# Kernel optimization log

Measured on AMD Instinct MI355X. Metric: run time of the kernel, lower is better.

## Reference

```python
import jax, jax.numpy as jnp
import numpy as np

N_HEAD = 16
N_KV_HEADS = 4
HEAD_SIZE = 128  # n_embd // n_head = 2048 // 16


def setup_inputs() -> dict:
    key = jax.random.key(0)
    k0, k1, k2 = jax.random.split(key, 3)
    B, T, C = 4, 2048, 2048
    kv_dim = N_KV_HEADS * HEAD_SIZE  # 512
    x = jax.random.normal(k0, (B, T, C), dtype=jnp.float32)
    W_attn = jax.random.normal(k1, (C, C + 2 * kv_dim), dtype=jnp.float32) * 0.02
    b_attn = jnp.zeros((C + 2 * kv_dim,), dtype=jnp.float32)
    W_proj = jax.random.normal(k2, (C, C), dtype=jnp.float32) * 0.02
    b_proj = jnp.zeros((C,), dtype=jnp.float32)
    return {"x": x, "W_attn": W_attn, "b_attn": b_attn, "W_proj": W_proj, "b_proj": b_proj}


def reference(x, W_attn, b_attn, W_proj, b_proj):
    B, T, C = x.shape
    hs = HEAD_SIZE
    kv_dim = N_KV_HEADS * hs
    qkv = x @ W_attn + b_attn                      # [B,T,C+2*kv_dim]
    q, k, v = jnp.split(qkv, [C, C + kv_dim], axis=2)
    q = q.reshape(B, T, N_HEAD, hs).transpose(0, 2, 1, 3)       # [B,H,T,hs]
    k = k.reshape(B, T, N_KV_HEADS, hs).transpose(0, 2, 1, 3)   # [B,Hkv,T,hs]
    v = v.reshape(B, T, N_KV_HEADS, hs).transpose(0, 2, 1, 3)
    # GQA: repeat_interleave kv heads to match query heads
    rep = N_HEAD // N_KV_HEADS
    k_r = jnp.repeat(k, rep, axis=1)               # [B,H,T,hs]
    v_r = jnp.repeat(v, rep, axis=1)
    scale = 1.0 / jnp.sqrt(jnp.float32(hs))
    scores = jnp.einsum('bhqd,bhkd->bhqk', q, k_r) * scale      # [B,H,T,T]
    causal = jnp.tril(jnp.ones((T, T), dtype=bool))
    scores = jnp.where(causal, scores, jnp.finfo(scores.dtype).min)
    attn = jax.nn.softmax(scores, axis=-1)
    y = jnp.einsum('bhqk,bhkd->bhqd', attn, v_r)   # [B,H,T,hs]
    y = y.transpose(0, 2, 1, 3).reshape(B, T, C)
    y = y @ W_proj + b_proj
    return y
```

## Files before the change

### kernel.cpp

```cpp
#include <hip/hip_runtime.h>
#include <stdint.h>

#define DEVI __device__ __forceinline__

typedef __attribute__((ext_vector_type(8))) uint16_t u16x8;
typedef __attribute__((ext_vector_type(4))) uint16_t u16x4v;
typedef __attribute__((ext_vector_type(4))) uint32_t u32x4;
typedef __attribute__((ext_vector_type(8))) __bf16 bf16x8;
typedef __attribute__((ext_vector_type(4))) float f32x4;
typedef __attribute__((ext_vector_type(16))) float f32x16;

DEVI uint16_t f2bf(float x) {
  union { float f; uint32_t u; } v; v.f = x;
  return (uint16_t)((v.u + 0x7fffu + ((v.u >> 16) & 1u)) >> 16);
}

DEVI uint16_t f2bfn(float f) {
  __bf16 h = (__bf16)f;
  return __builtin_bit_cast(uint16_t, h);
}

DEVI f32x4 mfma16(u16x8 a, u16x8 b, f32x4 c) {
  return __builtin_amdgcn_mfma_f32_16x16x32_bf16(
      __builtin_bit_cast(bf16x8, a), __builtin_bit_cast(bf16x8, b), c, 0, 0, 0);
}

DEVI f32x16 mfma32(u16x8 a, u16x8 b, f32x16 c) {
  return __builtin_amdgcn_mfma_f32_32x32x16_bf16(
      __builtin_bit_cast(bf16x8, a), __builtin_bit_cast(bf16x8, b), c, 0, 0, 0);
}

DEVI void async16(void* lds, const void* g) {
  __builtin_amdgcn_global_load_lds(
      (const __attribute__((address_space(1))) uint32_t*)g,
      (__attribute__((address_space(3))) uint32_t*)lds, 16, 0, 0);
}

#define QSC 0.12751742925f

__global__ void cvt_f32_bf16(const float* __restrict__ in, uint16_t* __restrict__ out, int n4) {
  int i = blockIdx.x * blockDim.x + threadIdx.x;
  const int st = gridDim.x * blockDim.x;
  for (; i < n4; i += st) {
    float4 v = ((const float4*)in)[i];
    u16x4v o;
    o[0] = f2bf(v.x); o[1] = f2bf(v.y); o[2] = f2bf(v.z); o[3] = f2bf(v.w);
    ((u16x4v*)out)[i] = o;
  }
}

__global__ void transp_cvt(const float* __restrict__ in, uint16_t* __restrict__ out,
                           int K, int N) {
  __shared__ float Ws[64][65];
  const int n0 = blockIdx.x * 64, k0 = blockIdx.y * 64;
  const int t = threadIdx.x;
  const int r = t >> 4, c = (t & 15) << 2;
#pragma unroll
  for (int it = 0; it < 4; ++it) {
    float4 v = *(const float4*)&in[(size_t)(k0 + it * 16 + r) * N + n0 + c];
    Ws[it * 16 + r][c] = v.x; Ws[it * 16 + r][c + 1] = v.y;
    Ws[it * 16 + r][c + 2] = v.z; Ws[it * 16 + r][c + 3] = v.w;
  }
  __syncthreads();
#pragma unroll
  for (int it = 0; it < 4; ++it) {
    const int rr = it * 16 + r;
    const int cc = c;
    ushort4 o;
    o.x = f2bf(Ws[cc][rr]);     o.y = f2bf(Ws[cc + 1][rr]);
    o.z = f2bf(Ws[cc + 2][rr]); o.w = f2bf(Ws[cc + 3][rr]);
    *(ushort4*)&out[(size_t)(n0 + rr) * K + k0 + cc] = o;
  }
}

__global__ __launch_bounds__(512, 1)
void gemm_qkv(const uint16_t* __restrict__ A, const uint16_t* __restrict__ Bt,
              const float* __restrict__ bias,
              uint16_t* __restrict__ q, uint16_t* __restrict__ kk, uint16_t* __restrict__ vt,
              int M, int N, int K) {
  constexpr int BK = 64;
  __shared__ uint16_t As[2][256 * BK];
  __shared__ uint16_t Bs[2][192 * BK];
  int bid = (int)blockIdx.x;
  const int q8 = (int)gridDim.x >> 3;
  bid = (bid & 7) * q8 + (bid >> 3);
  const int nbn = N / 192;
  const int brow = (bid / nbn) << 8;
  const int bcol = (bid % nbn) * 192;
  const int t = threadIdx.x;
  const int wid = t >> 6, lane = t & 63;
  const int wm = wid >> 1, wn = wid & 1;
  const int lr = lane & 15, g = lane >> 4, l7 = lr & 7;

  const int logch = (((t & 7) ^ ((t >> 3) & 7)) << 3);
  const uint16_t* Asrc = A + (size_t)(brow + (t >> 3)) * K + logch;
  const uint16_t* Bsrc = Bt + (size_t)(bcol + (t >> 3)) * K + logch;
  const size_t skip64 = (size_t)64 * K;
  const int dt = t * 8;

  auto stageA = [&](int buf, int k0) {
#pragma unroll
    for (int l = 0; l < 4; ++l)
      async16(&As[buf][l * 4096 + dt], Asrc + (size_t)l * skip64 + k0);
  };
  auto stageB = [&](int buf, int k0) {
#pragma unroll
    for (int l = 0; l < 3; ++l)
      async16(&Bs[buf][l * 4096 + dt], Bsrc + (size_t)l * skip64 + k0);
  };

  f32x4 acc[4][6];
#pragma unroll
  for (int i = 0; i < 4; ++i)
#pragma unroll
    for (int j = 0; j < 6; ++j) acc[i][j] = f32x4{0.f, 0.f, 0.f, 0.f};

  const int nt = K / BK;
  stageA(0, 0); stageB(0, 0);
  if (nt > 1) { stageA(1, BK); stageB(1, BK); }
  asm volatile("s_waitcnt vmcnt(0)" ::: "memory");
  __builtin_amdgcn_s_barrier();

  for (int tt = 0; tt < nt; ++tt) {
    const int buf = tt & 1;
    u16x8 bfr[6][2], af[4][2];
#pragma unroll
    for (int j = 0; j < 6; ++j) {
      const int brw = wn * 96 + j * 16 + lr;
#pragma unroll
      for (int s = 0; s < 2; ++s)
        bfr[j][s] = *(const u16x8*)&Bs[buf][brw * 64 + ((((s << 2) + g) ^ l7) << 3)];
    }
#pragma unroll
    for (int ii = 0; ii < 4; ++ii) {
      const int arow = wm * 64 + ii * 16 + lr;
#pragma unroll
      for (int s = 0; s < 2; ++s)
        af[ii][s] = *(const u16x8*)&As[buf][arow * 64 + ((((s << 2) + g) ^ l7) << 3)];
    }
    asm volatile("s_waitcnt lgkmcnt(0)" ::: "memory");
    __builtin_amdgcn_sched_barrier(0);
    __builtin_amdgcn_s_barrier();
    if (tt + 2 < nt) {
      stageA(buf, (tt + 2) * BK);
      stageB(buf, (tt + 2) * BK);
      asm volatile("s_waitcnt vmcnt(7)" ::: "memory");
    } else {
      asm volatile("s_waitcnt vmcnt(0)" ::: "memory");
    }
    __builtin_amdgcn_s_setprio(1);
#pragma unroll
    for (int ii = 0; ii < 4; ++ii)
#pragma unroll
      for (int j = 0; j < 6; ++j)
#pragma unroll
        for (int s = 0; s < 2; ++s)
          acc[ii][j] = mfma16(af[ii][s], bfr[j][s], acc[ii][j]);
    __builtin_amdgcn_s_setprio(0);
    __builtin_amdgcn_s_barrier();
  }

#pragma unroll
  for (int i = 0; i < 4; ++i) {
#pragma unroll
    for (int j = 0; j < 6; ++j) {
      const int col = bcol + wn * 96 + j * 16 + lr;
      const float bb = bias[col];
      const int rowb = brow + wm * 64 + i * 16 + (g << 2);
      const int b_ = rowb >> 11, ttb = rowb & 2047;
      const int d = col & 127;
      float vals[4];
#pragma unroll
      for (int r = 0; r < 4; ++r) vals[r] = acc[i][j][r] + bb;
      if (col < 2048) {
        const int hh = col >> 7;
#pragma unroll
        for (int r = 0; r < 4; ++r)
          q[((size_t)((b_ * 16 + hh) * 2048 + ttb + r) << 7) + d] = f2bf(vals[r] * QSC);
      } else if (col < 2560) {
        const int hh = (col - 2048) >> 7;
#pragma unroll
        for (int r = 0; r < 4; ++r)
          kk[((size_t)((b_ * 4 + hh) * 2048 + ttb + r) << 7) + d] = f2bf(vals[r]);
      } else {
        const int hh = (col - 2560) >> 7;
        u16x4v pk;
#pragma unroll
        for (int r = 0; r < 4; ++r) pk[r] = f2bf(vals[r]);
        *(u16x4v*)&vt[(((size_t)((b_ * 4 + hh) * 128 + d)) << 11) + ttb] = pk;
      }
    }
  }
}

__global__ __launch_bounds__(512, 1)
void gemm_proj(const uint16_t* __restrict__ A, const uint16_t* __restrict__ Bt,
               const float* __restrict__ bias, float* __restrict__ outF,
               int M, int N, int K) {
  constexpr int BK = 64;
  __shared__ uint16_t As[2][256 * BK];
  __shared__ uint16_t Bs[2][256 * BK];
  int bid = (int)blockIdx.x;
  const int q8 = (int)gridDim.x >> 3;
  bid = (bid & 7) * q8 + (bid >> 3);
  const int nbn = N >> 8;
  const int brow = (bid / nbn) << 8;
  const int bcol = (bid % nbn) << 8;
  const int t = threadIdx.x;
  const int wid = t >> 6, lane = t & 63;
  const int wm = wid >> 2, wn = wid & 3;
  const int lr = lane & 15, g = lane >> 4;
  const int l7 = lr & 7;

  const int sr0 = t >> 3;
  const int logch = (((t & 7) ^ ((t >> 3) & 7)) << 3);
  const uint16_t* Asrc0 = A + (size_t)(brow + sr0) * K + logch;
  const uint16_t* Asrc1 = A + (size_t)(brow + 64 + sr0) * K + logch;
  const uint16_t* Bsrc0 = Bt + (size_t)(bcol + sr0) * K + logch;
  const uint16_t* Bsrc1 = Bt + (size_t)(bcol + 64 + sr0) * K + logch;
  const size_t hskip = (size_t)128 * K;
  const int d0 = t * 8, d1 = 4096 + t * 8;

  auto stageA = [&](int buf, int k0) {
    async16(&As[buf][d0], Asrc0 + k0);
    async16(&As[buf][d1], Asrc1 + k0);
    async16(&As[buf][8192 + d0], Asrc0 + hskip + k0);
    async16(&As[buf][8192 + d1], Asrc1 + hskip + k0);
  };
  auto stageB = [&](int buf, int k0) {
    async16(&Bs[buf][d0], Bsrc0 + k0);
    async16(&Bs[buf][d1], Bsrc1 + k0);
    async16(&Bs[buf][8192 + d0], Bsrc0 + hskip + k0);
    async16(&Bs[buf][8192 + d1], Bsrc1 + hskip + k0);
  };

  f32x4 acc[8][4];
#pragma unroll
  for (int i = 0; i < 8; ++i)
#pragma unroll
    for (int j = 0; j < 4; ++j) acc[i][j] = f32x4{0.f, 0.f, 0.f, 0.f};

  const int nt = K / BK;
  stageA(0, 0); stageB(0, 0);
  if (nt > 1) stageB(1, BK);
  asm volatile("s_waitcnt vmcnt(0)" ::: "memory");
  __builtin_amdgcn_s_barrier();

  for (int tt = 0; tt < nt; ++tt) {
    const int buf = tt & 1;
    u16x8 bfr[4][2];
#pragma unroll
    for (int p = 0; p < 2; ++p) {
      if (p == 0) {
#pragma unroll
        for (int j = 0; j < 4; ++j) {
          const int brw = wn * 64 + j * 16 + lr;
#pragma unroll
          for (int s = 0; s < 2; ++s)
            bfr[j][s] = *(const u16x8*)&Bs[buf][brw * 64 + ((((s << 2) + g) ^ l7) << 3)];
        }
      }
      u16x8 af[4][2];
#pragma unroll
      for (int ii = 0; ii < 4; ++ii) {
        const int arow = wm * 128 + (p * 4 + ii) * 16 + lr;
#pragma unroll
        for (int s = 0; s < 2; ++s)
          af[ii][s] = *(const u16x8*)&As[buf][arow * 64 + ((((s << 2) + g) ^ l7) << 3)];
      }
      if (p == 0) {
        if (tt + 1 < nt) stageA(buf ^ 1, (tt + 1) * BK);
      } else {
        if (tt + 2 < nt) {
          stageB(buf, (tt + 2) * BK);
          asm volatile("s_waitcnt vmcnt(4)" ::: "memory");
        } else {
          asm volatile("s_waitcnt vmcnt(0)" ::: "memory");
        }
      }
      __builtin_amdgcn_s_barrier();
      __builtin_amdgcn_s_setprio(1);
#pragma unroll
      for (int ii = 0; ii < 4; ++ii)
#pragma unroll
        for (int j = 0; j < 4; ++j)
#pragma unroll
          for (int s = 0; s < 2; ++s)
            acc[p * 4 + ii][j] = mfma16(af[ii][s], bfr[j][s], acc[p * 4 + ii][j]);
      __builtin_amdgcn_s_setprio(0);
      __builtin_amdgcn_s_barrier();
    }
  }

#pragma unroll
  for (int i = 0; i < 8; ++i) {
#pragma unroll
    for (int j = 0; j < 4; ++j) {
      const int col = bcol + wn * 64 + j * 16 + lr;
      const float bb = bias[col];
#pragma unroll
      for (int r = 0; r < 4; ++r) {
        const int row = brow + wm * 128 + i * 16 + (g << 2) + r;
        outF[(size_t)row * N + col] = acc[i][j][r] + bb;
      }
    }
  }
}

__global__ __launch_bounds__(512, 1)
void attn_fwd(const uint16_t* __restrict__ Q,
              const uint16_t* __restrict__ Kg,
              const uint16_t* __restrict__ Vt,
              uint16_t* __restrict__ Y,
              int T) {
  __shared__ __align__(16) uint16_t Ks[2][64 * 128];
  __shared__ __align__(16) uint16_t Vs[128 * 64];
  const int id = (int)blockIdx.x;
  const int x = id & 7;
  const int h = (id >> 3) & 15, b = (id >> 7) & 3;
  const int qb = (id & 256) ? 7 - x : x;
  const int hkv = h >> 2;

  const int t = threadIdx.x, w = t >> 6, lane = t & 63;
  const int ql = lane & 31, b5 = lane >> 5;
  const int swzK = (ql & 15) << 3;
  const int swzV = (ql & 7) << 3;

  const uint16_t* Qp = Q + ((size_t)(b * 16 + h) * T + qb * 256) * 128;
  const uint16_t* Kp = Kg + (size_t)(b * 4 + hkv) * T * 128;
  const uint16_t* Vp = Vt + (size_t)(b * 4 + hkv) * 128 * T;

  auto stageK = [&](int buf, int kv0) {
#pragma unroll
    for (int l = 0; l < 2; ++l) {
      const int s = l * 512 + t;
      const int row = s >> 4;
      const int cl = (s & 15) ^ (row & 15);
      async16(&Ks[buf][s * 8], &Kp[(size_t)(kv0 + row) * 128 + cl * 8]);
    }
  };
  auto stageV = [&](int kv0) {
#pragma unroll
    for (int l = 0; l < 2; ++l) {
      const int s = l * 512 + t;
      const int row = s >> 3;
      const int cl = (s & 7) ^ (row & 7);
      async16(&Vs[s * 8], &Vp[(size_t)row * T + kv0 + cl * 8]);
    }
  };

  const int row0 = qb * 256 + w * 32;
  const int qrow = row0 + ql;

  u16x8 qf[8];
#pragma unroll
  for (int kc = 0; kc < 8; ++kc)
    qf[kc] = *(const u16x8*)&Qp[(size_t)(w * 32 + ql) * 128 + kc * 16 + b5 * 8];

  f32x16 o[4];
#pragma unroll
  for (int db = 0; db < 4; ++db)
#pragma unroll
    for (int r = 0; r < 16; ++r) o[db][r] = 0.f;
  float mrow = -3e38f, lrow = 0.f;

  const int ntiles = 4 * qb + 4;
  const int myn = 4 * qb + (w >> 1) + 1;

  stageK(0, 0);
  __syncthreads();

  int cur = 0;
  for (int tile = 0; tile < ntiles; ++tile) {
    const int kv0 = tile << 6;
    stageV(kv0);
    if (tile + 1 < ntiles) stageK(cur ^ 1, (tile + 1) << 6);

    const bool run = tile < myn;
    f32x16 s[2];
    u16x8 pa[4];
    if (run) {
#pragma unroll
      for (int m = 0; m < 2; ++m)
#pragma unroll
        for (int r = 0; r < 16; ++r) s[m][r] = 0.f;
      __builtin_amdgcn_s_setprio(1);
#pragma unroll
      for (int kc = 0; kc < 8; ++kc) {
        const int cc = (kc * 16 + b5 * 8) ^ swzK;
        u16x8 k0f = *(const u16x8*)&Ks[cur][ql * 128 + cc];
        u16x8 k1f = *(const u16x8*)&Ks[cur][(32 + ql) * 128 + cc];
        s[0] = mfma32(k0f, qf[kc], s[0]);
        s[1] = mfma32(k1f, qf[kc], s[1]);
      }
      __builtin_amdgcn_s_setprio(0);

      if (kv0 + 63 > row0) {
#pragma unroll
        for (int m = 0; m < 2; ++m)
#pragma unroll
          for (int r = 0; r < 16; ++r) {
            const int kg = kv0 + 32 * m + (r & 3) + 8 * (r >> 2) + 4 * b5;
            if (kg > qrow) s[m][r] = -3e38f;
          }
      }
      float mt[16];
#pragma unroll
      for (int r = 0; r < 16; ++r) mt[r] = fmaxf(s[0][r], s[1][r]);
#pragma unroll
      for (int st = 8; st >= 1; st >>= 1)
#pragma unroll
        for (int r = 0; r < st; ++r) mt[r] = fmaxf(mt[r], mt[r + st]);
      float mx = fmaxf(mt[0], __shfl_xor(mt[0], 32));
      const bool defer = __all(mx <= mrow + 8.f);
      const float mnew = defer ? mrow : fmaxf(mrow, mx);
      const float sc = defer ? 1.f : exp2f(mrow - mnew);
#pragma unroll
      for (int m = 0; m < 2; ++m)
#pragma unroll
        for (int r = 0; r < 16; ++r) s[m][r] = exp2f(s[m][r] - mnew);
      float pt[16];
#pragma unroll
      for (int r = 0; r < 16; ++r) pt[r] = s[0][r] + s[1][r];
#pragma unroll
      for (int st = 8; st >= 1; st >>= 1)
#pragma unroll
        for (int r = 0; r < st; ++r) pt[r] += pt[r + st];
      float ps = pt[0] + __shfl_xor(pt[0], 32);
      mrow = mnew;
      lrow = lrow * sc + ps;
      if (!defer) {
#pragma unroll
        for (int db = 0; db < 4; ++db)
#pragma unroll
          for (int r = 0; r < 16; ++r) o[db][r] *= sc;
      }

#pragma unroll
      for (int m = 0; m < 2; ++m) {
        uint32_t pw[4][2];
#pragma unroll
        for (int a = 0; a < 4; ++a)
#pragma unroll
          for (int hh = 0; hh < 2; ++hh)
            pw[a][hh] = (uint32_t)f2bfn(s[m][4 * a + 2 * hh]) |
                        ((uint32_t)f2bfn(s[m][4 * a + 2 * hh + 1]) << 16);
#pragma unroll
        for (int c = 0; c < 2; ++c) {
          uint32_t wd[4];
#pragma unroll
          for (int hh = 0; hh < 2; ++hh) {
            const uint32_t mine  = b5 ? pw[2 * c + 1][hh] : pw[2 * c][hh];
            const uint32_t yours = b5 ? pw[2 * c][hh] : pw[2 * c + 1][hh];
            const uint32_t xw = (uint32_t)__shfl_xor((int)yours, 32);
            wd[hh] = b5 ? xw : mine;
            wd[2 + hh] = b5 ? mine : xw;
          }
          u32x4 tmp = {wd[0], wd[1], wd[2], wd[3]};
          pa[2 * m + c] = __builtin_bit_cast(u16x8, tmp);
        }
      }
    }
    __syncthreads();

    if (run) {
      __builtin_amdgcn_s_setprio(1);
#pragma unroll
      for (int db = 0; db < 4; ++db) {
#pragma unroll
        for (int kf = 0; kf < 4; ++kf) {
          u16x8 vf = *(const u16x8*)&Vs[(32 * db + ql) * 64 +
                                        ((kf * 16 + b5 * 8) ^ swzV)];
          o[db] = mfma32(vf, pa[kf], o[db]);
        }
      }
      __builtin_amdgcn_s_setprio(0);
    }
    __syncthreads();
    cur ^= 1;
  }

  uint16_t* Yp = Y + ((size_t)(b * T + row0 + ql)) * 2048 + h * 128 + b5 * 4;
  const float inv = 1.f / lrow;
#pragma unroll
  for (int db = 0; db < 4; ++db)
#pragma unroll
    for (int a = 0; a < 4; ++a) {
      u16x4v pk;
#pragma unroll
      for (int r = 0; r < 4; ++r) pk[r] = f2bfn(o[db][4 * a + r] * inv);
      *(u16x4v*)&Yp[db * 32 + a * 8] = pk;
    }
}

extern "C" void kernel_launch(void* const* d_in, const int* in_sizes, int n_in,
                              void* d_out, int out_size, void* d_ws, size_t ws_size,
                              hipStream_t stream) {
  const float* x      = (const float*)d_in[0];
  const float* W_attn = (const float*)d_in[1];
  const float* b_attn = (const float*)d_in[2];
  const float* W_proj = (const float*)d_in[3];
  const float* b_proj = (const float*)d_in[4];
  float* out = (float*)d_out;

  const int B = 4, T = 2048, C = 2048, H = 16, HKV = 4, HS = 128;
  const int M = B * T;
  const int Nqkv = C + 2 * HKV * HS;

  uint8_t* ws = (uint8_t*)d_ws;
  size_t off = 0;
  auto alloc = [&](size_t bytes) {
    void* p = ws + off;
    off += (bytes + 255) & ~(size_t)255;
    return p;
  };
  uint16_t* xb  = (uint16_t*)alloc((size_t)M * C * 2);
  uint16_t* WaT = (uint16_t*)alloc((size_t)Nqkv * C * 2);
  uint16_t* WpT = (uint16_t*)alloc((size_t)C * C * 2);
  uint16_t* qb  = (uint16_t*)alloc((size_t)B * H * T * HS * 2);
  uint16_t* kb  = (uint16_t*)alloc((size_t)B * HKV * T * HS * 2);
  uint16_t* vtb = (uint16_t*)alloc((size_t)B * HKV * HS * T * 2);
  uint16_t* yb  = xb;

  cvt_f32_bf16<<<2048, 256, 0, stream>>>(x, xb, M * C / 4);
  transp_cvt<<<dim3(Nqkv / 64, C / 64), 256, 0, stream>>>(W_attn, WaT, C, Nqkv);
  transp_cvt<<<dim3(C / 64, C / 64), 256, 0, stream>>>(W_proj, WpT, C, C);
  gemm_qkv<<<dim3((M / 256) * (Nqkv / 192)), 512, 0, stream>>>(
      xb, WaT, b_attn, qb, kb, vtb, M, Nqkv, C);
  attn_fwd<<<dim3(512), 512, 0, stream>>>(qb, kb, vtb, yb, T);
  gemm_proj<<<dim3((M / 256) * (C / 256)), 512, 0, stream>>>(
      yb, WpT, b_proj, out, M, C, C);
}
```

Baseline: 319.4 us.

## Software-pipeline attention loop: overlap QK^T of next tile with softmax+PV of previous

Result: faster. 308.3 us, median of 2 (-3.5%).

```diff
diff --git a/kernel.cpp b/kernel.cpp
--- a/kernel.cpp
+++ b/kernel.cpp
@@ -314,7 +314,7 @@
               uint16_t* __restrict__ Y,
               int T) {
   __shared__ __align__(16) uint16_t Ks[2][64 * 128];
-  __shared__ __align__(16) uint16_t Vs[128 * 64];
+  __shared__ __align__(16) uint16_t Vs[2][128 * 64];
   const int id = (int)blockIdx.x;
   const int x = id & 7;
   const int h = (id >> 3) & 15, b = (id >> 7) & 3;
@@ -339,13 +339,13 @@
       async16(&Ks[buf][s * 8], &Kp[(size_t)(kv0 + row) * 128 + cl * 8]);
     }
   };
-  auto stageV = [&](int kv0) {
+  auto stageV = [&](int buf, int kv0) {
 #pragma unroll
     for (int l = 0; l < 2; ++l) {
       const int s = l * 512 + t;
       const int row = s >> 3;
       const int cl = (s & 7) ^ (row & 7);
-      async16(&Vs[s * 8], &Vp[(size_t)row * T + kv0 + cl * 8]);
+      async16(&Vs[buf][s * 8], &Vp[(size_t)row * T + kv0 + cl * 8]);
     }
   };
 
@@ -367,118 +367,121 @@
   const int ntiles = 4 * qb + 4;
   const int myn = 4 * qb + (w >> 1) + 1;
 
+  auto qk = [&](int tp, f32x16* sp) {
+    sp[0] = 0.f; sp[1] = 0.f;
+    const int kbuf = tp & 1;
+    __builtin_amdgcn_s_setprio(1);
+#pragma unroll
+    for (int kc = 0; kc < 8; ++kc) {
+      const int cc = (kc * 16 + b5 * 8) ^ swzK;
+      u16x8 k0f = *(const u16x8*)&Ks[kbuf][ql * 128 + cc];
+      u16x8 k1f = *(const u16x8*)&Ks[kbuf][(32 + ql) * 128 + cc];
+      sp[0] = mfma32(k0f, qf[kc], sp[0]);
+      sp[1] = mfma32(k1f, qf[kc], sp[1]);
+    }
+    __builtin_amdgcn_s_setprio(0);
+  };
+
+  auto finish = [&](int tp, f32x16* sp) {
+    const int kv0 = tp << 6;
+    if (kv0 + 63 > row0) {
+#pragma unroll
+      for (int m = 0; m < 2; ++m)
+#pragma unroll
+        for (int r = 0; r < 16; ++r) {
+          const int kg = kv0 + 32 * m + (r & 3) + 8 * (r >> 2) + 4 * b5;
+          if (kg > qrow) sp[m][r] = -3e38f;
+        }
+    }
+    float mt[16];
+#pragma unroll
+    for (int r = 0; r < 16; ++r) mt[r] = fmaxf(sp[0][r], sp[1][r]);
+#pragma unroll
+    for (int st = 8; st >= 1; st >>= 1)
+#pragma unroll
+      for (int r = 0; r < st; ++r) mt[r] = fmaxf(mt[r], mt[r + st]);
+    float mx = fmaxf(mt[0], __shfl_xor(mt[0], 32));
+    const bool defer = __all(mx <= mrow + 8.f);
+    const float mnew = defer ? mrow : fmaxf(mrow, mx);
+    const float sc = defer ? 1.f : exp2f(mrow - mnew);
+#pragma unroll
+    for (int m = 0; m < 2; ++m)
+#pragma unroll
+      for (int r = 0; r < 16; ++r) sp[m][r] = exp2f(sp[m][r] - mnew);
+    float pt[16];
+#pragma unroll
+    for (int r = 0; r < 16; ++r) pt[r] = sp[0][r] + sp[1][r];
+#pragma unroll
+    for (int st = 8; st >= 1; st >>= 1)
+#pragma unroll
+      for (int r = 0; r < st; ++r) pt[r] += pt[r + st];
+    float ps = pt[0] + __shfl_xor(pt[0], 32);
+    mrow = mnew;
+    lrow = lrow * sc + ps;
+    if (!defer) {
+#pragma unroll
+      for (int db = 0; db < 4; ++db)
+#pragma unroll
+        for (int r = 0; r < 16; ++r) o[db][r] *= sc;
+    }
+    u16x8 pa[4];
+#pragma unroll
+    for (int m = 0; m < 2; ++m) {
+      uint32_t pw[4][2];
+#pragma unroll
+      for (int a = 0; a < 4; ++a)
+#pragma unroll
+        for (int hh = 0; hh < 2; ++hh)
+          pw[a][hh] = (uint32_t)f2bfn(sp[m][4 * a + 2 * hh]) |
+                      ((uint32_t)f2bfn(sp[m][4 * a + 2 * hh + 1]) << 16);
+#pragma unroll
+      for (int c = 0; c < 2; ++c) {
+        uint32_t wd[4];
+#pragma unroll
+        for (int hh = 0; hh < 2; ++hh) {
+          const uint32_t mine  = b5 ? pw[2 * c + 1][hh] : pw[2 * c][hh];
+          const uint32_t yours = b5 ? pw[2 * c][hh] : pw[2 * c + 1][hh];
+          const uint32_t xw = (uint32_t)__shfl_xor((int)yours, 32);
+          wd[hh] = b5 ? xw : mine;
+          wd[2 + hh] = b5 ? mine : xw;
+        }
+        u32x4 tmp = {wd[0], wd[1], wd[2], wd[3]};
+        pa[2 * m + c] = __builtin_bit_cast(u16x8, tmp);
+      }
+    }
+    const int vbuf = tp & 1;
+    __builtin_amdgcn_s_setprio(1);
+#pragma unroll
+    for (int db = 0; db < 4; ++db) {
+#pragma unroll
+      for (int kf = 0; kf < 4; ++kf) {
+        u16x8 vf = *(const u16x8*)&Vs[vbuf][(32 * db + ql) * 64 +
+                                           ((kf * 16 + b5 * 8) ^ swzV)];
+        o[db] = mfma32(vf, pa[kf], o[db]);
+      }
+    }
+    __builtin_amdgcn_s_setprio(0);
+  };
+
+  f32x16 sA[2], sB[2];
+
   stageK(0, 0);
   __syncthreads();
 
-  int cur = 0;
-  for (int tile = 0; tile < ntiles; ++tile) {
-    const int kv0 = tile << 6;
-    stageV(kv0);
-    if (tile + 1 < ntiles) stageK(cur ^ 1, (tile + 1) << 6);
-
-    const bool run = tile < myn;
-    f32x16 s[2];
-    u16x8 pa[4];
-    if (run) {
-#pragma unroll
-      for (int m = 0; m < 2; ++m)
-#pragma unroll
-        for (int r = 0; r < 16; ++r) s[m][r] = 0.f;
-      __builtin_amdgcn_s_setprio(1);
-#pragma unroll
-      for (int kc = 0; kc < 8; ++kc) {
-        const int cc = (kc * 16 + b5 * 8) ^ swzK;
-        u16x8 k0f = *(const u16x8*)&Ks[cur][ql * 128 + cc];
-        u16x8 k1f = *(const u16x8*)&Ks[cur][(32 + ql) * 128 + cc];
-        s[0] = mfma32(k0f, qf[kc], s[0]);
-        s[1] = mfma32(k1f, qf[kc], s[1]);
-      }
-      __builtin_amdgcn_s_setprio(0);
-
-      if (kv0 + 63 > row0) {
-#pragma unroll
-        for (int m = 0; m < 2; ++m)
-#pragma unroll
-          for (int r = 0; r < 16; ++r) {
-            const int kg = kv0 + 32 * m + (r & 3) + 8 * (r >> 2) + 4 * b5;
-            if (kg > qrow) s[m][r] = -3e38f;
-          }
-      }
-      float mt[16];
-#pragma unroll
-      for (int r = 0; r < 16; ++r) mt[r] = fmaxf(s[0][r], s[1][r]);
-#pragma unroll
-      for (int st = 8; st >= 1; st >>= 1)
-#pragma unroll
-        for (int r = 0; r < st; ++r) mt[r] = fmaxf(mt[r], mt[r + st]);
-      float mx = fmaxf(mt[0], __shfl_xor(mt[0], 32));
-      const bool defer = __all(mx <= mrow + 8.f);
-      const float mnew = defer ? mrow : fmaxf(mrow, mx);
-      const float sc = defer ? 1.f : exp2f(mrow - mnew);
-#pragma unroll
-      for (int m = 0; m < 2; ++m)
-#pragma unroll
-        for (int r = 0; r < 16; ++r) s[m][r] = exp2f(s[m][r] - mnew);
-      float pt[16];
-#pragma unroll
-      for (int r = 0; r < 16; ++r) pt[r] = s[0][r] + s[1][r];
-#pragma unroll
-      for (int st = 8; st >= 1; st >>= 1)
-#pragma unroll
-        for (int r = 0; r < st; ++r) pt[r] += pt[r + st];
-      float ps = pt[0] + __shfl_xor(pt[0], 32);
-      mrow = mnew;
-      lrow = lrow * sc + ps;
-      if (!defer) {
-#pragma unroll
-        for (int db = 0; db < 4; ++db)
-#pragma unroll
-          for (int r = 0; r < 16; ++r) o[db][r] *= sc;
-      }
-
-#pragma unroll
-      for (int m = 0; m < 2; ++m) {
-        uint32_t pw[4][2];
-#pragma unroll
-        for (int a = 0; a < 4; ++a)
-#pragma unroll
-          for (int hh = 0; hh < 2; ++hh)
-            pw[a][hh] = (uint32_t)f2bfn(s[m][4 * a + 2 * hh]) |
-                        ((uint32_t)f2bfn(s[m][4 * a + 2 * hh + 1]) << 16);
-#pragma unroll
-        for (int c = 0; c < 2; ++c) {
-          uint32_t wd[4];
-#pragma unroll
-          for (int hh = 0; hh < 2; ++hh) {
-            const uint32_t mine  = b5 ? pw[2 * c + 1][hh] : pw[2 * c][hh];
-            const uint32_t yours = b5 ? pw[2 * c][hh] : pw[2 * c + 1][hh];
-            const uint32_t xw = (uint32_t)__shfl_xor((int)yours, 32);
-            wd[hh] = b5 ? xw : mine;
-            wd[2 + hh] = b5 ? mine : xw;
-          }
-          u32x4 tmp = {wd[0], wd[1], wd[2], wd[3]};
-          pa[2 * m + c] = __builtin_bit_cast(u16x8, tmp);
-        }
-      }
-    }
+  for (int tile = 0; tile < ntiles; tile += 2) {
+    stageV(0, tile << 6);
+    if (tile + 1 < ntiles) stageK(1, (tile + 1) << 6);
+    if (tile < myn) qk(tile, sA);
+    if (tile >= 1 && tile - 1 < myn) finish(tile - 1, sB);
     __syncthreads();
-
-    if (run) {
-      __builtin_amdgcn_s_setprio(1);
-#pragma unroll
-      for (int db = 0; db < 4; ++db) {
-#pragma unroll
-        for (int kf = 0; kf < 4; ++kf) {
-          u16x8 vf = *(const u16x8*)&Vs[(32 * db + ql) * 64 +
-                                        ((kf * 16 + b5 * 8) ^ swzV)];
-          o[db] = mfma32(vf, pa[kf], o[db]);
-        }
-      }
-      __builtin_amdgcn_s_setprio(0);
-    }
+    const int t2 = tile + 1;
+    stageV(1, t2 << 6);
+    if (t2 + 1 < ntiles) stageK(0, (t2 + 1) << 6);
+    if (t2 < myn) qk(t2, sB);
+    if (t2 - 1 < myn) finish(t2 - 1, sA);
     __syncthreads();
-    cur ^= 1;
-  }
+  }
+  if (ntiles - 1 < myn) finish(ntiles - 1, sB);
 
   uint16_t* Yp = Y + ((size_t)(b * T + row0 + ql)) * 2048 + h * 128 + b5 * 4;
   const float inv = 1.f / lrow;
```
